# Optimization experiments

Measured on AMD Instinct MI355X. Metric: run time of the kernel, lower is better.

## Reference

```python
import jax, jax.numpy as jnp
import numpy as np

N_NODES = 50000
N_EDGES = 800000
D = 64  # in_dim = hidden = out_dim
LEAKY_SLOPE = 0.01  # F.leaky_relu default


def gat_layer(h, src, dst, W, b, aW, ab):
    # fc: z = h @ W.T + b            [N, D_out]
    z = h @ W.T + b
    zs = z[src]                       # gather src feats  [E, D_out]
    zd = z[dst]                       # gather dst feats  [E, D_out]
    # attn_fc(concat(z_src, z_dst)) -> scalar per edge, then leaky_relu
    e = jnp.concatenate([zs, zd], axis=-1) @ aW.T + ab   # [E, 1]
    e = jax.nn.leaky_relu(e, LEAKY_SLOPE)[:, 0]          # [E]
    # softmax over incoming edges per destination node (mailbox softmax)
    m = jax.ops.segment_max(e, dst, num_segments=N_NODES)    # [N]
    ex = jnp.exp(e - m[dst])
    den = jax.ops.segment_sum(ex, dst, num_segments=N_NODES)  # [N]
    alpha = ex / den[dst]                                      # [E]
    # scatter-sum aggregate of alpha * z_src
    return jax.ops.segment_sum(alpha[:, None] * zs, dst, num_segments=N_NODES)


def setup_inputs() -> dict:
    key = jax.random.key(0)
    ks = jax.random.split(key, 16)
    x = jax.random.normal(ks[0], (N_NODES, D), dtype=jnp.float32)
    src = jax.random.randint(ks[1], (N_EDGES,), 0, N_NODES)
    dst = jax.random.randint(ks[2], (N_EDGES,), 0, N_NODES)
    # xavier_normal with relu gain, per reset_parameters
    gain = float(np.sqrt(2.0))
    params = {}
    for i in range(3):
        std_fc = gain * np.sqrt(2.0 / (D + D))
        std_at = gain * np.sqrt(2.0 / (2 * D + 1))
        params[f"W{i}"] = jax.random.normal(ks[3 + 4 * i], (D, D), dtype=jnp.float32) * std_fc
        params[f"b{i}"] = jnp.zeros((D,), dtype=jnp.float32)
        params[f"a{i}"] = jax.random.normal(ks[4 + 4 * i], (1, 2 * D), dtype=jnp.float32) * std_at
        params[f"ab{i}"] = jnp.zeros((1,), dtype=jnp.float32)
    return {"x": x, "src": src, "dst": dst, **params}


def reference(x, src, dst, W0, b0, a0, ab0, W1, b1, a1, ab1, W2, b2, a2, ab2):
    h = gat_layer(x, src, dst, W0, b0, a0, ab0)
    h = jax.nn.relu(h)
    h = gat_layer(h, src, dst, W1, b1, a1, ab1)
    h = jax.nn.relu(h)
    h = gat_layer(h, src, dst, W2, b2, a2, ab2)
    return h
```

## Files before the change

kernel.cpp:

```cpp
#include <hip/hip_runtime.h>
#include <math.h>

#define N_NODES 50000
#define N_EDGES 800000
#define D 64

#define NB 256
#define NBLK 256
#define BUCKET_NODES 196
#define TILE 3125

typedef unsigned short ushort_t;

__device__ __forceinline__ ushort_t f32_to_bf16(float f) {
    unsigned u = __float_as_uint(f);
    u += 0x7fffu + ((u >> 16) & 1u);
    return (ushort_t)(u >> 16);
}
__device__ __forceinline__ unsigned fkey(float f) {
    unsigned b = __float_as_uint(f);
    return (b & 0x80000000u) ? ~b : (b | 0x80000000u);
}
__device__ __forceinline__ float funkey(unsigned u) {
    unsigned b = (u & 0x80000000u) ? (u ^ 0x80000000u) : ~u;
    return __uint_as_float(b);
}

template<int N>
__global__ void scan_partial_g(const int* __restrict__ in, int* __restrict__ partials) {
    const int base = blockIdx.x * 1024 + threadIdx.x * 4;
    int4 c = make_int4(0, 0, 0, 0);
    if (base + 3 < N) c = *(const int4*)&in[base];
    else { int* cp = (int*)&c; for (int j = 0; j < 4; ++j) if (base + j < N) cp[j] = in[base + j]; }
    int s = c.x + c.y + c.z + c.w;
    #pragma unroll
    for (int off = 32; off >= 1; off >>= 1) s += __shfl_xor(s, off, 64);
    __shared__ int red[4];
    if ((threadIdx.x & 63) == 0) red[threadIdx.x >> 6] = s;
    __syncthreads();
    if (threadIdx.x == 0) partials[blockIdx.x] = red[0] + red[1] + red[2] + red[3];
}

template<int N, int NT>
__global__ void scan_write_i(const int* __restrict__ in, const int* __restrict__ partials_raw,
                             int* __restrict__ out) {
    __shared__ int toff;
    __shared__ int sh[256];
    const int tid = threadIdx.x;
    if (tid < 64) {
        const int v = (tid < NT) ? partials_raw[tid] : 0;
        int inc = v;
        #pragma unroll
        for (int off = 1; off < 64; off <<= 1) {
            const int w = __shfl_up(inc, off, 64);
            if (tid >= off) inc += w;
        }
        if (tid == blockIdx.x) toff = inc - v;
    }
    const int base = blockIdx.x * 1024 + tid * 4;
    int4 c = make_int4(0, 0, 0, 0);
    if (base + 3 < N) c = *(const int4*)&in[base];
    else { int* cp = (int*)&c; for (int j = 0; j < 4; ++j) if (base + j < N) cp[j] = in[base + j]; }
    const int s = c.x + c.y + c.z + c.w;
    sh[tid] = s;
    __syncthreads();
    for (int off = 1; off < 256; off <<= 1) {
        const int w = (tid >= off) ? sh[tid - off] : 0;
        __syncthreads();
        sh[tid] += w;
        __syncthreads();
    }
    int run = toff + sh[tid] - s;
    const int* cp = (const int*)&c;
    int rp[4];
    #pragma unroll
    for (int j = 0; j < 4; ++j) { rp[j] = run; run += cp[j]; }
    if (base + 3 < N) *(int4*)&out[base] = make_int4(rp[0], rp[1], rp[2], rp[3]);
    else for (int j = 0; j < 4; ++j) if (base + j < N) out[base + j] = rp[j];
}

__global__ __launch_bounds__(256) void bucket_hist(const int* __restrict__ dst,
                                                   int* __restrict__ Acnt) {
    __shared__ int hist[NB];
    for (int i = threadIdx.x; i < NB; i += 256) hist[i] = 0;
    __syncthreads();
    const int base = blockIdx.x * TILE;
    for (int i = threadIdx.x; i < TILE; i += 256)
        atomicAdd(&hist[dst[base + i] / BUCKET_NODES], 1);
    __syncthreads();
    for (int bk = threadIdx.x; bk < NB; bk += 256)
        Acnt[bk * NBLK + blockIdx.x] = hist[bk];
}

__global__ __launch_bounds__(256) void bucket_scatter(const int* __restrict__ src,
                                                      const int* __restrict__ dst,
                                                      const int* __restrict__ offs,
                                                      int2* __restrict__ staging) {
    __shared__ int cur[NB];
    for (int i = threadIdx.x; i < NB; i += 256) cur[i] = offs[i * NBLK + blockIdx.x];
    __syncthreads();
    const int base = blockIdx.x * TILE;
    for (int i = threadIdx.x; i < TILE; i += 256) {
        const int s = src[base + i], d = dst[base + i];
        const int pos = atomicAdd(&cur[d / BUCKET_NODES], 1);
        staging[pos] = make_int2(s, d);
    }
}

__global__ __launch_bounds__(256) void node_counts(const int2* __restrict__ staging,
                                                   const int* __restrict__ offs,
                                                   int* __restrict__ counts,
                                                   int* __restrict__ bucket_sum) {
    __shared__ int cnt[BUCKET_NODES];
    __shared__ int red[4];
    const int b = blockIdx.x, tid = threadIdx.x;
    for (int i = tid; i < BUCKET_NODES; i += 256) cnt[i] = 0;
    __syncthreads();
    const int s0 = offs[b * NBLK];
    const int s1 = (b == NB - 1) ? N_EDGES : offs[(b + 1) * NBLK];
    for (int i = s0 + tid; i < s1; i += 256)
        atomicAdd(&cnt[staging[i].y - b * BUCKET_NODES], 1);
    __syncthreads();
    for (int i = tid; i < BUCKET_NODES; i += 256) {
        const int node = b * BUCKET_NODES + i;
        if (node < N_NODES) counts[node] = cnt[i];
    }
    int s = (tid < BUCKET_NODES) ? cnt[tid] : 0;
    #pragma unroll
    for (int off = 32; off >= 1; off >>= 1) s += __shfl_xor(s, off, 64);
    if ((tid & 63) == 0) red[tid >> 6] = s;
    __syncthreads();
    if (tid == 0) bucket_sum[b] = red[0] + red[1] + red[2] + red[3];
}

__global__ __launch_bounds__(256) void row_ptr_build(const int* __restrict__ counts,
                                                     const int* __restrict__ bucket_sum,
                                                     int* __restrict__ row_ptr) {
    __shared__ int bs[NB];
    __shared__ int loc[256];
    const int b = blockIdx.x, tid = threadIdx.x;
    bs[tid] = bucket_sum[tid];
    __syncthreads();
    for (int off = 1; off < 256; off <<= 1) {
        const int w = (tid >= off) ? bs[tid - off] : 0;
        __syncthreads();
        bs[tid] += w;
        __syncthreads();
    }
    const int bucket_off = bs[b] - bucket_sum[b];
    const int node = b * BUCKET_NODES + tid;
    const int c = (tid < BUCKET_NODES && node < N_NODES) ? counts[node] : 0;
    loc[tid] = c;
    __syncthreads();
    for (int off = 1; off < 256; off <<= 1) {
        const int w = (tid >= off) ? loc[tid - off] : 0;
        __syncthreads();
        loc[tid] += w;
        __syncthreads();
    }
    if (tid < BUCKET_NODES && node < N_NODES) row_ptr[node] = bucket_off + loc[tid] - c;
    if (b == 0 && tid == 0) row_ptr[N_NODES] = N_EDGES;
}

__global__ __launch_bounds__(256) void bucket_to_csr(const int2* __restrict__ staging,
                                                     const int* __restrict__ offs,
                                                     const int* __restrict__ row_ptr,
                                                     int* __restrict__ csr_src) {
    __shared__ int cur[BUCKET_NODES];
    const int b = blockIdx.x;
    for (int i = threadIdx.x; i < BUCKET_NODES; i += 256) {
        const int node = b * BUCKET_NODES + i;
        cur[i] = (node < N_NODES) ? row_ptr[node] : 0;
    }
    __syncthreads();
    const int s0 = offs[b * NBLK];
    const int s1 = (b == NB - 1) ? N_EDGES : offs[(b + 1) * NBLK];
    for (int i = s0 + threadIdx.x; i < s1; i += 256) {
        const int2 e = staging[i];
        const int pos = atomicAdd(&cur[e.y - b * BUCKET_NODES], 1);
        csr_src[pos] = e.x;
    }
}

#define NL_ROWS 8
__global__ __launch_bounds__(256) void node_linear_gemm(
    const float* __restrict__ h, ushort_t* __restrict__ zb,
    const float* __restrict__ W, const float* __restrict__ b,
    const float* __restrict__ a, const float* __restrict__ ab,
    float* __restrict__ s_src, float* __restrict__ s_dst)
{
    __shared__ float Wt[64 * 65];
    for (int idx = threadIdx.x; idx < D * D; idx += 256) {
        const int j = idx >> 6, k = idx & 63;
        Wt[k * 65 + j] = W[idx];
    }
    __syncthreads();

    const int lane = threadIdx.x & 63;
    const int wv   = __builtin_amdgcn_readfirstlane(threadIdx.x >> 6);
    const int row0 = (blockIdx.x * 4 + wv) * NL_ROWS;
    if (row0 >= N_NODES) return;

    const float bj  = b[lane];
    const float alo = a[lane];
    const float ahi = a[64 + lane];

    const float* hr[NL_ROWS];
    #pragma unroll
    for (int r = 0; r < NL_ROWS; ++r) hr[r] = h + (size_t)(row0 + r) * D;

    float acc[NL_ROWS];
    #pragma unroll
    for (int r = 0; r < NL_ROWS; ++r) acc[r] = bj;

    #pragma unroll 4
    for (int k = 0; k < D; ++k) {
        const float wkj = Wt[k * 65 + lane];
        #pragma unroll
        for (int r = 0; r < NL_ROWS; ++r)
            acc[r] = fmaf(hr[r][k], wkj, acc[r]);
    }

    #pragma unroll
    for (int r = 0; r < NL_ROWS; ++r) {
        zb[(size_t)(row0 + r) * D + lane] = f32_to_bf16(acc[r]);
        float u = acc[r] * alo;
        float v = acc[r] * ahi;
        #pragma unroll
        for (int off = 32; off >= 1; off >>= 1) {
            u += __shfl_xor(u, off, 64);
            v += __shfl_xor(v, off, 64);
        }
        if (lane == 0) { s_src[row0 + r] = u; s_dst[row0 + r] = v + ab[0]; }
    }
}

__global__ __launch_bounds__(256) void reduce_smax(const float* __restrict__ s_src,
                                                   unsigned* __restrict__ gmax_u) {
    __shared__ float red[4];
    const int tid = blockIdx.x * 256 + threadIdx.x;
    float m = -INFINITY;
    if (tid * 4 + 3 < N_NODES) {
        const float4 v = *(const float4*)&s_src[tid * 4];
        m = fmaxf(fmaxf(v.x, v.y), fmaxf(v.z, v.w));
    } else {
        for (int j = tid * 4; j < min(tid * 4 + 4, N_NODES); ++j) m = fmaxf(m, s_src[j]);
    }
    #pragma unroll
    for (int off = 32; off >= 1; off >>= 1) m = fmaxf(m, __shfl_xor(m, off, 64));
    if ((threadIdx.x & 63) == 0) red[threadIdx.x >> 6] = m;
    __syncthreads();
    if (threadIdx.x == 0) {
        m = fmaxf(fmaxf(red[0], red[1]), fmaxf(red[2], red[3]));
        atomicMax(gmax_u, fkey(m));
    }
}

template<bool RELU>
__global__ __launch_bounds__(256) void fused_gather_ub(
    const int* __restrict__ row_ptr, const int* __restrict__ csr_src,
    const float* __restrict__ s_src, const float* __restrict__ s_dst,
    const unsigned* __restrict__ gmax_u,
    const ushort_t* __restrict__ zb, float* __restrict__ out)
{
    __shared__ int2 sh[4][4][64];
    const int lane = threadIdx.x & 63;
    const int wv   = __builtin_amdgcn_readfirstlane(threadIdx.x >> 6);
    const int node0 = (blockIdx.x * 4 + wv) * 4;
    if (node0 >= N_NODES) return;
    const float gmax = funkey(*gmax_u);

    int begq[4], endq[4];
    float sdq[4], mubq[4];
    int maxdeg = 0;
    #pragma unroll
    for (int q = 0; q < 4; ++q) {
        begq[q] = row_ptr[node0 + q];
        endq[q] = row_ptr[node0 + q + 1];
        sdq[q]  = s_dst[node0 + q];
        const float mu = gmax + sdq[q];
        mubq[q] = mu > 0.f ? mu : 0.01f * mu;
        maxdeg = max(maxdeg, endq[q] - begq[q]);
    }

    const int half = lane >> 5;
    const int fl   = lane & 31;
    float2 acc[4][2];
    float denl[4];
    #pragma unroll
    for (int q = 0; q < 4; ++q) {
        acc[q][0] = make_float2(0.f, 0.f);
        acc[q][1] = make_float2(0.f, 0.f);
        denl[q] = 0.f;
    }

    for (int c = 0; c < maxdeg; c += 64) {
        #pragma unroll
        for (int q = 0; q < 4; ++q) {
            int2 ws = make_int2(0, 0);
            const int i = begq[q] + c + lane;
            if (i < endq[q]) {
                const int s = csr_src[i];
                float e = s_src[s] + sdq[q];
                e = e > 0.f ? e : 0.01f * e;
                const float w = __expf(e - mubq[q]);
                denl[q] += w;
                ws = make_int2(__float_as_int(w), s);
            }
            sh[wv][q][lane] = ws;
        }
        const int n = min(64, maxdeg - c);
        for (int t = 0; t < n; t += 4) {
            #pragma unroll
            for (int q = 0; q < 4; ++q) {
                const int2 wa = sh[wv][q][t + half];
                const int2 wb = sh[wv][q][t + 2 + half];
                const unsigned ua = *(const unsigned*)&zb[(size_t)wa.y * D + 2 * fl];
                const unsigned ub = *(const unsigned*)&zb[(size_t)wb.y * D + 2 * fl];
                const float fa = __int_as_float(wa.x);
                const float fb = __int_as_float(wb.x);
                acc[q][0].x = fmaf(fa, __uint_as_float(ua << 16), acc[q][0].x);
                acc[q][0].y = fmaf(fa, __uint_as_float(ua & 0xffff0000u), acc[q][0].y);
                acc[q][1].x = fmaf(fb, __uint_as_float(ub << 16), acc[q][1].x);
                acc[q][1].y = fmaf(fb, __uint_as_float(ub & 0xffff0000u), acc[q][1].y);
            }
        }
    }
    #pragma unroll
    for (int q = 0; q < 4; ++q) {
        float den = denl[q];
        #pragma unroll
        for (int off = 32; off >= 1; off >>= 1) den += __shfl_xor(den, off, 64);
        float2 tot = make_float2(acc[q][0].x + acc[q][1].x,
                                 acc[q][0].y + acc[q][1].y);
        tot.x += __shfl_xor(tot.x, 32, 64);
        tot.y += __shfl_xor(tot.y, 32, 64);
        const float inv = (den > 0.f) ? 1.f / den : 0.f;
        float2 v = make_float2(tot.x * inv, tot.y * inv);
        if (RELU) { v.x = fmaxf(v.x, 0.f); v.y = fmaxf(v.y, 0.f); }
        if (half == 0)
            *(float2*)&out[(size_t)(node0 + q) * D + 2 * fl] = v;
    }
}

extern "C" void kernel_launch(void* const* d_in, const int* in_sizes, int n_in,
                              void* d_out, int out_size, void* d_ws, size_t ws_size,
                              hipStream_t stream) {
    const float* x   = (const float*)d_in[0];
    const int*   src = (const int*)d_in[1];
    const int*   dst = (const int*)d_in[2];
    float* out = (float*)d_out;

    char* wp = (char*)d_ws;
    auto alloc = [&](size_t bytes) -> void* {
        void* p = (void*)wp;
        wp += (bytes + 255) & ~(size_t)255;
        return p;
    };
    ushort_t* zb      = (ushort_t*)alloc((size_t)N_NODES * D * sizeof(ushort_t));
    float* s_src      = (float*)alloc((size_t)N_NODES * sizeof(float));
    float* s_dst      = (float*)alloc((size_t)N_NODES * sizeof(float));
    int*   counts     = (int*)alloc((size_t)N_NODES * sizeof(int));
    int*   row_ptr    = (int*)alloc((size_t)(N_NODES + 1) * sizeof(int));
    int*   csr_src    = (int*)alloc((size_t)N_EDGES * sizeof(int));
    int*   partB      = (int*)alloc(64 * sizeof(int));
    int*   bucket_sum = (int*)alloc((size_t)NB * sizeof(int));
    unsigned* gmax_u  = (unsigned*)alloc(4 * sizeof(unsigned));
    int*   Acnt       = (int*)alloc((size_t)NB * NBLK * sizeof(int));
    int*   offs       = (int*)alloc((size_t)NB * NBLK * sizeof(int));
    int2*  staging    = (int2*)alloc((size_t)N_EDGES * sizeof(int2));
    (void)ws_size;

    hipMemsetAsync(gmax_u, 0, 4 * sizeof(unsigned), stream);

    bucket_hist<<<NBLK, 256, 0, stream>>>(dst, Acnt);
    scan_partial_g<NB * NBLK><<<64, 256, 0, stream>>>(Acnt, partB);
    scan_write_i<NB * NBLK, 64><<<64, 256, 0, stream>>>(Acnt, partB, offs);
    bucket_scatter<<<NBLK, 256, 0, stream>>>(src, dst, offs, staging);
    node_counts<<<NB, 256, 0, stream>>>(staging, offs, counts, bucket_sum);
    row_ptr_build<<<NB, 256, 0, stream>>>(counts, bucket_sum, row_ptr);
    bucket_to_csr<<<NB, 256, 0, stream>>>(staging, offs, row_ptr, csr_src);

    const int grid_k1 = (N_NODES + 4 * NL_ROWS - 1) / (4 * NL_ROWS);
    const int grid_fg = N_NODES / 16;

    for (int layer = 0; layer < 3; ++layer) {
        const float* W  = (const float*)d_in[3 + 4 * layer];
        const float* b  = (const float*)d_in[4 + 4 * layer];
        const float* a  = (const float*)d_in[5 + 4 * layer];
        const float* ab = (const float*)d_in[6 + 4 * layer];
        const float* hin = (layer == 0) ? x : out;

        node_linear_gemm<<<grid_k1, 256, 0, stream>>>(hin, zb, W, b, a, ab, s_src, s_dst);
        reduce_smax<<<64, 256, 0, stream>>>(s_src, &gmax_u[layer]);
        if (layer < 2) {
            fused_gather_ub<true ><<<grid_fg, 256, 0, stream>>>(row_ptr, csr_src, s_src, s_dst,
                                                                &gmax_u[layer], zb, out);
        } else {
            fused_gather_ub<false><<<grid_fg, 256, 0, stream>>>(row_ptr, csr_src, s_src, s_dst,
                                                                &gmax_u[layer], zb, out);
        }
    }
}
```

Before: 204.8 us.

## Sort destination nodes by in-degree to balance gather wave workloads

Adds a counting sort of nodes by in-degree (histogram, scan, scatter) that produces a permutation. The fused gather kernel then processes nodes in permuted order so the four nodes sharing a wave have similar degrees, which cuts idle lanes caused by maxdeg divergence. The cost is four extra small kernel launches plus one indirection per node and scattered output writes.

New measurement: 218.9 us, median of 4. 1.07x slower.

```diff
diff --git a/kernel.cpp b/kernel.cpp
--- a/kernel.cpp
+++ b/kernel.cpp
@@ -9,6 +9,8 @@
 #define NBLK 256
 #define BUCKET_NODES 196
 #define TILE 3125
+#define DBIN 256
+#define DBLK 49
 
 typedef unsigned short ushort_t;
 
@@ -182,6 +184,37 @@
     }
 }
 
+__global__ __launch_bounds__(256) void deg_hist(const int* __restrict__ counts,
+                                                int* __restrict__ Dcnt) {
+    __shared__ int hist[DBIN];
+    for (int i = threadIdx.x; i < DBIN; i += 256) hist[i] = 0;
+    __syncthreads();
+    const int base = blockIdx.x * 1024;
+    for (int i = threadIdx.x; i < 1024; i += 256) {
+        const int node = base + i;
+        if (node < N_NODES) atomicAdd(&hist[min(counts[node], DBIN - 1)], 1);
+    }
+    __syncthreads();
+    for (int bk = threadIdx.x; bk < DBIN; bk += 256)
+        Dcnt[bk * DBLK + blockIdx.x] = hist[bk];
+}
+
+__global__ __launch_bounds__(256) void perm_scatter(const int* __restrict__ counts,
+                                                    const int* __restrict__ Doffs,
+                                                    int* __restrict__ perm) {
+    __shared__ int cur[DBIN];
+    for (int i = threadIdx.x; i < DBIN; i += 256) cur[i] = Doffs[i * DBLK + blockIdx.x];
+    __syncthreads();
+    const int base = blockIdx.x * 1024;
+    for (int i = threadIdx.x; i < 1024; i += 256) {
+        const int node = base + i;
+        if (node < N_NODES) {
+            const int pos = atomicAdd(&cur[min(counts[node], DBIN - 1)], 1);
+            perm[pos] = node;
+        }
+    }
+}
+
 #define NL_ROWS 8
 __global__ __launch_bounds__(256) void node_linear_gemm(
     const float* __restrict__ h, ushort_t* __restrict__ zb,
@@ -258,6 +291,7 @@
 
 template<bool RELU>
 __global__ __launch_bounds__(256) void fused_gather_ub(
+    const int* __restrict__ perm,
     const int* __restrict__ row_ptr, const int* __restrict__ csr_src,
     const float* __restrict__ s_src, const float* __restrict__ s_dst,
     const unsigned* __restrict__ gmax_u,
@@ -266,18 +300,19 @@
     __shared__ int2 sh[4][4][64];
     const int lane = threadIdx.x & 63;
     const int wv   = __builtin_amdgcn_readfirstlane(threadIdx.x >> 6);
-    const int node0 = (blockIdx.x * 4 + wv) * 4;
-    if (node0 >= N_NODES) return;
+    const int pbase = (blockIdx.x * 4 + wv) * 4;
+    if (pbase >= N_NODES) return;
     const float gmax = funkey(*gmax_u);
 
-    int begq[4], endq[4];
+    int nq[4], begq[4], endq[4];
     float sdq[4], mubq[4];
     int maxdeg = 0;
     #pragma unroll
     for (int q = 0; q < 4; ++q) {
-        begq[q] = row_ptr[node0 + q];
-        endq[q] = row_ptr[node0 + q + 1];
-        sdq[q]  = s_dst[node0 + q];
+        nq[q]   = perm[pbase + q];
+        begq[q] = row_ptr[nq[q]];
+        endq[q] = row_ptr[nq[q] + 1];
+        sdq[q]  = s_dst[nq[q]];
         const float mu = gmax + sdq[q];
         mubq[q] = mu > 0.f ? mu : 0.01f * mu;
         maxdeg = max(maxdeg, endq[q] - begq[q]);
@@ -339,7 +374,7 @@
         float2 v = make_float2(tot.x * inv, tot.y * inv);
         if (RELU) { v.x = fmaxf(v.x, 0.f); v.y = fmaxf(v.y, 0.f); }
         if (half == 0)
-            *(float2*)&out[(size_t)(node0 + q) * D + 2 * fl] = v;
+            *(float2*)&out[(size_t)nq[q] * D + 2 * fl] = v;
     }
 }
 
@@ -363,9 +398,13 @@
     int*   counts     = (int*)alloc((size_t)N_NODES * sizeof(int));
     int*   row_ptr    = (int*)alloc((size_t)(N_NODES + 1) * sizeof(int));
     int*   csr_src    = (int*)alloc((size_t)N_EDGES * sizeof(int));
+    int*   perm       = (int*)alloc((size_t)N_NODES * sizeof(int));
     int*   partB      = (int*)alloc(64 * sizeof(int));
+    int*   partC      = (int*)alloc(64 * sizeof(int));
     int*   bucket_sum = (int*)alloc((size_t)NB * sizeof(int));
     unsigned* gmax_u  = (unsigned*)alloc(4 * sizeof(unsigned));
+    int*   Dcnt       = (int*)alloc((size_t)DBIN * DBLK * sizeof(int));
+    int*   Doffs      = (int*)alloc((size_t)DBIN * DBLK * sizeof(int));
     int*   Acnt       = (int*)alloc((size_t)NB * NBLK * sizeof(int));
     int*   offs       = (int*)alloc((size_t)NB * NBLK * sizeof(int));
     int2*  staging    = (int2*)alloc((size_t)N_EDGES * sizeof(int2));
@@ -381,6 +420,11 @@
     row_ptr_build<<<NB, 256, 0, stream>>>(counts, bucket_sum, row_ptr);
     bucket_to_csr<<<NB, 256, 0, stream>>>(staging, offs, row_ptr, csr_src);
 
+    deg_hist<<<DBLK, 256, 0, stream>>>(counts, Dcnt);
+    scan_partial_g<DBIN * DBLK><<<13, 256, 0, stream>>>(Dcnt, partC);
+    scan_write_i<DBIN * DBLK, 13><<<13, 256, 0, stream>>>(Dcnt, partC, Doffs);
+    perm_scatter<<<DBLK, 256, 0, stream>>>(counts, Doffs, perm);
+
     const int grid_k1 = (N_NODES + 4 * NL_ROWS - 1) / (4 * NL_ROWS);
     const int grid_fg = N_NODES / 16;
 
@@ -394,10 +438,10 @@
         node_linear_gemm<<<grid_k1, 256, 0, stream>>>(hin, zb, W, b, a, ab, s_src, s_dst);
         reduce_smax<<<64, 256, 0, stream>>>(s_src, &gmax_u[layer]);
         if (layer < 2) {
-            fused_gather_ub<true ><<<grid_fg, 256, 0, stream>>>(row_ptr, csr_src, s_src, s_dst,
+            fused_gather_ub<true ><<<grid_fg, 256, 0, stream>>>(perm, row_ptr, csr_src, s_src, s_dst,
                                                                 &gmax_u[layer], zb, out);
         } else {
-            fused_gather_ub<false><<<grid_fg, 256, 0, stream>>>(row_ptr, csr_src, s_src, s_dst,
+            fused_gather_ub<false><<<grid_fg, 256, 0, stream>>>(perm, row_ptr, csr_src, s_src, s_dst,
                                                                 &gmax_u[layer], zb, out);
         }
     }
```
